# Kernel optimization log

Measured on AMD Instinct MI355X. Metric: run time of the kernel, lower is better.

Reference implementation:

```python
import jax, jax.numpy as jnp
import numpy as np
from jax import lax

V_VOX, T_PTS, D, H, W = 12000, 35, 10, 200, 176
EPS = 1e-5


def _bn(x, g, b, axes, shape):
    m = x.mean(axes, keepdims=True)
    v = x.var(axes, keepdims=True)  # biased var, matches torch BN training stats
    return g.reshape(shape) * (x - m) * lax.rsqrt(v + EPS) + b.reshape(shape)


def _conv3d(x, w, b):
    y = lax.conv_general_dilated(x, w, (1, 1, 1), 'SAME',
                                 dimension_numbers=('NCDHW', 'OIDHW', 'NCDHW'))
    return y + b[None, :, None, None, None]


def _conv2d(x, w, b):
    y = lax.conv_general_dilated(x, w, (1, 1), 'SAME',
                                 dimension_numbers=('NCHW', 'OIHW', 'NCHW'))
    return y + b[None, :, None, None]


def setup_inputs() -> dict:
    key = jax.random.key(0)
    ks = jax.random.split(key, 12)
    voxels = jax.random.normal(ks[0], (1, V_VOX, T_PTS, 4), jnp.float32)
    # unique voxel coordinates (the torch loop overwrites on duplicates; unique avoids ambiguity)
    rng = np.random.default_rng(0)
    flat = rng.choice(D * H * W, size=V_VOX, replace=False)
    z = flat // (H * W); rem = flat % (H * W)
    coords = jnp.asarray(np.stack([z, rem // W, rem % W], axis=1), dtype=jnp.int32)
    s = 0.05
    p = dict(
        w_lin=jax.random.normal(ks[1], (32, 4), jnp.float32) * s,
        b_lin=jnp.zeros((32,), jnp.float32),
        g_bn0=jnp.ones((32,), jnp.float32), be_bn0=jnp.zeros((32,), jnp.float32),
        w_c3a=jax.random.normal(ks[2], (64, 32, 3, 3, 3), jnp.float32) * s,
        b_c3a=jnp.zeros((64,), jnp.float32),
        g_bn1=jnp.ones((64,), jnp.float32), be_bn1=jnp.zeros((64,), jnp.float32),
        w_c3b=jax.random.normal(ks[3], (64, 64, 3, 3, 3), jnp.float32) * s,
        b_c3b=jnp.zeros((64,), jnp.float32),
        g_bn2=jnp.ones((64,), jnp.float32), be_bn2=jnp.zeros((64,), jnp.float32),
        w_r1=jax.random.normal(ks[4], (128, 64, 3, 3), jnp.float32) * s,
        b_r1=jnp.zeros((128,), jnp.float32),
        w_r2=jax.random.normal(ks[5], (8, 128, 1, 1), jnp.float32) * s,
        b_r2=jnp.zeros((8,), jnp.float32),
    )
    return dict(voxels=voxels, coords=coords, **p)


def reference(voxels, coords, w_lin, b_lin, g_bn0, be_bn0,
              w_c3a, b_c3a, g_bn1, be_bn1, w_c3b, b_c3b, g_bn2, be_bn2,
              w_r1, b_r1, w_r2, b_r2):
    B, V, T, C = voxels.shape
    # SimpleVFE: linear -> BN1d (batch stats) -> relu -> max over points
    h = voxels.reshape(B * V * T, C) @ w_lin.T + b_lin          # [BVT,32]
    h = jax.nn.relu(_bn(h, g_bn0, be_bn0, 0, (1, 32)))
    feats = h.reshape(B, V, T, 32).max(axis=2)                  # [B,V,32]
    # fused scatter into dense volume (replaces per-voxel python loop)
    volume = jnp.zeros((B, 32, D, H, W), voxels.dtype)
    volume = volume.at[0, :, coords[:, 0], coords[:, 1], coords[:, 2]].set(feats[0])
    # 3D backbone
    x = jax.nn.relu(_bn(_conv3d(volume, w_c3a, b_c3a), g_bn1, be_bn1, (0, 2, 3, 4), (1, 64, 1, 1, 1)))
    x = jax.nn.relu(_bn(_conv3d(x, w_c3b, b_c3b), g_bn2, be_bn2, (0, 2, 3, 4), (1, 64, 1, 1, 1)))
    x = x.mean(axis=2)                                          # collapse depth -> [B,64,H,W]
    # RPN head
    out = _conv2d(jax.nn.relu(_conv2d(x, w_r1, b_r1)), w_r2, b_r2)  # [B,8,H,W]
    box = jnp.concatenate([out[:, 0:3], jnp.exp(out[:, 3:6]),
                           jnp.tanh(out[:, 6:7]), jax.nn.sigmoid(out[:, 7:8])], axis=1)
    return box
```

## Files before the change

### kernel.cpp

```cpp
#include <hip/hip_runtime.h>
#include <math.h>

#define V_VOX 12000
#define T_PTS 35
#define DD 10
#define HH 200
#define WW 176
#define EPSV 1e-5f

#define DP 12
#define HP 202
#define WP 178
#define PPLN (HP * WP)
#define PVOX (DP * PPLN)
#define NPIX (DD * HH * WW)
#define HWPIX (HH * WW)

typedef _Float16 half_t;
typedef _Float16 f16x8 __attribute__((ext_vector_type(8)));
typedef float f32x4 __attribute__((ext_vector_type(4)));

#define WPA_OFF 0
#define WPB_OFF 110592
#define WPR1_OFF 331776
#define STATS_OFF 479232
#define FEATS_OFF 483328
#define VOLP_OFF 2019328
#define X1P_OFF 29633536
#define Y_OFF 84861952
#define PLANE_OFF 129917952
#define R1OUT_OFF 134520320

#define S_BN0S 0
#define S_BN0Q 32
#define S_BN1S 64
#define S_BN1Q 128
#define S_BN2S 192
#define S_BN2Q 256
#define C0A 320
#define C0B 352
#define C1A 384
#define C1B 448
#define C2A 512
#define C2B 576

__device__ __forceinline__ void gload16(const half_t* g, half_t* l) {
    __builtin_amdgcn_global_load_lds(
        (const __attribute__((address_space(1))) void*)g,
        (__attribute__((address_space(3))) void*)l, 16, 0, 0);
}

__global__ void k_pack(const float* __restrict__ w, half_t* __restrict__ wp,
                       int IC, int NT, int OC) {
    int id = blockIdx.x * 256 + threadIdx.x;
    int OCT = OC >> 4, KH = IC >> 5;
    int total = NT * KH * OCT * 512;
    if (id >= total) return;
    int j = id & 7;
    int lane = (id >> 3) & 63;
    int rest = id >> 9;
    int ot = rest % OCT; rest /= OCT;
    int kh = rest % KH;
    int tap = rest / KH;
    int oc = ot * 16 + (lane & 15);
    int ic = kh * 32 + (lane >> 4) * 8 + j;
    wp[id] = (half_t)w[(oc * IC + ic) * NT + tap];
}

__global__ void k_vfe_stats(const float4* __restrict__ vox, const float* __restrict__ w_lin,
                            const float* __restrict__ b_lin, float* __restrict__ S) {
    int tid = blockIdx.x * 256 + threadIdx.x;
    int c = threadIdx.x & 31;
    float4 w = ((const float4*)w_lin)[c];
    float bl = b_lin[c];
    float s = 0.f, q = 0.f;
    const int np = V_VOX * T_PTS;
    int stride = gridDim.x * 8;
    for (int p = tid >> 5; p < np; p += stride) {
        float4 v = vox[p];
        float d = v.x * w.x + v.y * w.y + v.z * w.z + v.w * w.w + bl;
        s += d;
        q += d * d;
    }
    s += __shfl_xor(s, 32);
    q += __shfl_xor(q, 32);
    if ((threadIdx.x & 63) < 32) {
        atomicAdd(&S[S_BN0S + c], s);
        atomicAdd(&S[S_BN0Q + c], q);
    }
}

__global__ void k_bn_final(const float* __restrict__ ss, const float* __restrict__ sq,
                           const float* __restrict__ g, const float* __restrict__ be,
                           float* __restrict__ ca, float* __restrict__ cb, int C, float invN) {
    int c = threadIdx.x;
    if (c >= C) return;
    float m = ss[c] * invN;
    float v = sq[c] * invN - m * m;
    float a = g[c] * rsqrtf(v + EPSV);
    ca[c] = a;
    cb[c] = be[c] - m * a;
}

__global__ void k_vfe_max(const float4* __restrict__ vox, const float* __restrict__ w_lin,
                          const float* __restrict__ b_lin, const float* __restrict__ ca,
                          const float* __restrict__ cb, float* __restrict__ feats) {
    int id = blockIdx.x * 256 + threadIdx.x;
    if (id >= V_VOX * 32) return;
    int c = id & 31;
    int v = id >> 5;
    float4 w = ((const float4*)w_lin)[c];
    float bl = b_lin[c], A = ca[c], B = cb[c];
    float m = 0.f;
    for (int t = 0; t < T_PTS; t++) {
        float4 p = vox[v * T_PTS + t];
        float d = p.x * w.x + p.y * w.y + p.z * w.z + p.w * w.w + bl;
        m = fmaxf(m, A * d + B);
    }
    feats[id] = m;
}

__global__ void k_scatter(const float* __restrict__ feats, const int* __restrict__ coords,
                          half_t* __restrict__ volp) {
    int id = blockIdx.x * 256 + threadIdx.x;
    if (id >= V_VOX * 32) return;
    int c = id & 31;
    int v = id >> 5;
    int z = coords[v * 3 + 0];
    int y = coords[v * 3 + 1];
    int x = coords[v * 3 + 2];
    volp[(((z + 1) * HP + (y + 1)) * WP + (x + 1)) * 32 + c] = (half_t)feats[id];
}

template <int KH, int DZ, int OCTP, bool RELU, bool STATS>
__global__ __launch_bounds__(256, 3) void k_conv(const half_t* __restrict__ in,
                                                 size_t khstride,
                                                 const half_t* __restrict__ wp,
                                                 const float* __restrict__ bias,
                                                 half_t* __restrict__ out,
                                                 float* __restrict__ ssum,
                                                 float* __restrict__ ssq) {
    constexpr int OC = OCTP * 16;
    constexpr int NS = DZ * KH;
    __shared__ __align__(16) half_t tA[2][24 * 512];

    const int tid = threadIdx.x;
    const int lane = tid & 63;
    const int wv = tid >> 6;
    const int x0 = blockIdx.x * 16;
    const int y0b = blockIdx.y * 16;
    const int bz = blockIdx.z;
    const int z0 = (DZ == 3) ? (bz >> 1) : 0;
    const int ocb = (DZ == 3) ? (bz & 1) * 2 : bz * 2;
    const int y0w = y0b + wv * 4;
    const bool valid = (y0w < HH);
    const int colc = lane & 15, grp = lane >> 4;

    unsigned gofsA[6];
#pragma unroll
    for (int i = 0; i < 6; ++i) {
        int run = wv + 4 * i;
        int c = run * 64 + lane;
        if (c > 1295) c = 1295;
        int pixhi = c >> 3, s = c & 7;
        int b = ((s >> 2) ^ (pixhi >> 1)) & 1;
        int q = ((s ^ b) & 1) | ((((s >> 1) ^ pixhi) & 1) << 1);
        int pix = pixhi * 2 + b;
        int row = pix / 18, px = pix - row * 18;
        int srow = y0b + row;
        if (srow > HP - 1) srow = HP - 1;
        gofsA[i] = (unsigned)((srow * WP + x0 + px) * 32 + q * 8);
    }

    f32x4 acc[4][2];
#pragma unroll
    for (int m = 0; m < 4; m++)
#pragma unroll
        for (int n = 0; n < 2; n++) acc[m][n] = (f32x4)(0.f);

    auto STAGEA = [&](int s, int buf) {
        const int dz = s / KH, kh = s % KH;
        const half_t* sl = in + (size_t)kh * khstride
                           + (size_t)(z0 + dz) * (DZ == 3 ? (size_t)PPLN * 32 : 0);
#pragma unroll
        for (int i = 0; i < 6; ++i) {
            int run = wv + 4 * i;
            gload16(sl + gofsA[i], &tA[buf][run * 512]);
        }
    };

    STAGEA(0, 0);

#pragma unroll 1
    for (int s = 0; s < NS; ++s) {
        const int dz = s / KH, kh = s % KH;
        f16x8 Breg[9][2];
#pragma unroll
        for (int tap = 0; tap < 9; ++tap)
#pragma unroll
            for (int n = 0; n < 2; ++n)
                Breg[tap][n] = *(const f16x8*)(wp
                    + (((size_t)(dz * 9 + tap) * KH + kh) * OCTP + ocb + n) * 512 + lane * 8);
        asm volatile("" ::: "memory");
        if (s + 1 < NS) {
            STAGEA(s + 1, (s + 1) & 1);
            asm volatile("s_waitcnt vmcnt(6)" ::: "memory");
        } else {
            asm volatile("s_waitcnt vmcnt(0)" ::: "memory");
        }
        __builtin_amdgcn_s_barrier();

        if (valid) {
            const int buf = s & 1;
#pragma unroll
            for (int dx = 0; dx < 3; ++dx) {
                f16x8 Af[6];
#pragma unroll
                for (int r = 0; r < 6; ++r) {
                    int pix = (wv * 4 + r) * 18 + colc + dx;
                    int ah = ((pix << 5) | (grp << 3)) ^ ((pix & 7) << 3);
                    Af[r] = *(const f16x8*)&tA[buf][ah];
                }
#pragma unroll
                for (int dy = 0; dy < 3; ++dy)
#pragma unroll
                    for (int m = 0; m < 4; ++m)
#pragma unroll
                        for (int n = 0; n < 2; ++n)
                            acc[m][n] = __builtin_amdgcn_mfma_f32_16x16x32_f16(
                                Af[dy + m], Breg[dy * 3 + dx][n], acc[m][n], 0, 0, 0);
            }
        }
        asm volatile("s_waitcnt lgkmcnt(0)" ::: "memory");
        __builtin_amdgcn_s_barrier();
    }

    if (!valid) return;
#pragma unroll
    for (int n = 0; n < 2; ++n) {
        int oc = (ocb + n) * 16 + colc;
        float bv = bias[oc];
        float s = 0.f, q = 0.f;
#pragma unroll
        for (int m = 0; m < 4; ++m) {
            int yy = y0w + m;
#pragma unroll
            for (int i = 0; i < 4; ++i) {
                int xx = x0 + grp * 4 + i;
                float v = acc[m][n][i] + bv;
                if (STATS) { s += v; q += v * v; }
                float w = RELU ? fmaxf(v, 0.f) : v;
                out[((size_t)(z0 * HH + yy) * WW + xx) * OC + oc] = (half_t)w;
            }
        }
        if (STATS) {
            s += __shfl_xor(s, 16); s += __shfl_xor(s, 32);
            q += __shfl_xor(q, 16); q += __shfl_xor(q, 32);
            if (lane < 16) {
                atomicAdd(&ssum[oc], s);
                atomicAdd(&ssq[oc], q);
            }
        }
    }
}

__global__ void k_activate(const half_t* __restrict__ y1, const float* __restrict__ ca,
                           const float* __restrict__ cb, half_t* __restrict__ xp) {
    int id = blockIdx.x * 256 + threadIdx.x;
    if (id >= PVOX * 8) return;
    int c0 = (id & 7) * 8;
    int pix = id >> 3;
    int zp = pix / PPLN;
    int rem = pix - zp * PPLN;
    int yp = rem / WP;
    int xq = rem - yp * WP;
    f16x8 o;
    if (zp >= 1 && zp <= DD && yp >= 1 && yp <= HH && xq >= 1 && xq <= WW) {
        size_t p = ((size_t)((zp - 1) * HH + (yp - 1)) * WW + (xq - 1));
        f16x8 v = *(const f16x8*)(y1 + p * 64 + c0);
#pragma unroll
        for (int j = 0; j < 8; j++)
            o[j] = (half_t)fmaxf(ca[c0 + j] * (float)v[j] + cb[c0 + j], 0.f);
    } else {
#pragma unroll
        for (int j = 0; j < 8; j++) o[j] = (half_t)0.f;
    }
    int khp = c0 >> 5;
    *(f16x8*)(xp + (size_t)khp * PVOX * 32 + (size_t)pix * 32 + (c0 & 31)) = o;
}

__global__ void k_depthmean(const half_t* __restrict__ y2, const float* __restrict__ ca,
                            const float* __restrict__ cb, half_t* __restrict__ plane) {
    int id = blockIdx.x * 256 + threadIdx.x;
    int c = id & 63;
    int pix = id >> 6;
    int yp = pix / WP;
    int xq = pix - yp * WP;
    float val = 0.f;
    if (yp >= 1 && yp <= HH && xq >= 1 && xq <= WW) {
        float A = ca[c], B = cb[c], s = 0.f;
        const half_t* base = y2 + ((size_t)(yp - 1) * WW + (xq - 1)) * 64 + c;
#pragma unroll
        for (int z = 0; z < DD; z++)
            s += fmaxf(A * (float)base[(size_t)z * HWPIX * 64] + B, 0.f);
        val = s * 0.1f;
    }
    int khp = c >> 5;
    plane[(size_t)khp * PPLN * 32 + (size_t)pix * 32 + (c & 31)] = (half_t)val;
}

__global__ void k_r2(const half_t* __restrict__ r1o, const float* __restrict__ w,
                     const float* __restrict__ bias, float* __restrict__ outp) {
    __shared__ float wsm[1024];
    for (int i = threadIdx.x; i < 1024; i += 256) wsm[i] = w[i];
    __syncthreads();
    int p = blockIdx.x * 256 + threadIdx.x;
    if (p >= HWPIX) return;
    float acc[8];
#pragma unroll
    for (int o = 0; o < 8; o++) acc[o] = bias[o];
    const half_t* rb = r1o + (size_t)p * 128;
#pragma unroll 4
    for (int icb = 0; icb < 128; icb += 8) {
        f16x8 v = *(const f16x8*)(rb + icb);
#pragma unroll
        for (int j = 0; j < 8; j++) {
            float vv = (float)v[j];
#pragma unroll
            for (int o = 0; o < 8; o++) acc[o] += vv * wsm[o * 128 + icb + j];
        }
    }
    outp[0 * HWPIX + p] = acc[0];
    outp[1 * HWPIX + p] = acc[1];
    outp[2 * HWPIX + p] = acc[2];
    outp[3 * HWPIX + p] = expf(acc[3]);
    outp[4 * HWPIX + p] = expf(acc[4]);
    outp[5 * HWPIX + p] = expf(acc[5]);
    outp[6 * HWPIX + p] = tanhf(acc[6]);
    outp[7 * HWPIX + p] = 1.f / (1.f + expf(-acc[7]));
}

extern "C" void kernel_launch(void* const* d_in, const int* in_sizes, int n_in,
                              void* d_out, int out_size, void* d_ws, size_t ws_size,
                              hipStream_t stream) {
    const float4* voxels = (const float4*)d_in[0];
    const int* coords = (const int*)d_in[1];
    const float* w_lin = (const float*)d_in[2];
    const float* b_lin = (const float*)d_in[3];
    const float* g_bn0 = (const float*)d_in[4];
    const float* be_bn0 = (const float*)d_in[5];
    const float* w_c3a = (const float*)d_in[6];
    const float* b_c3a = (const float*)d_in[7];
    const float* g_bn1 = (const float*)d_in[8];
    const float* be_bn1 = (const float*)d_in[9];
    const float* w_c3b = (const float*)d_in[10];
    const float* b_c3b = (const float*)d_in[11];
    const float* g_bn2 = (const float*)d_in[12];
    const float* be_bn2 = (const float*)d_in[13];
    const float* w_r1 = (const float*)d_in[14];
    const float* b_r1 = (const float*)d_in[15];
    const float* w_r2 = (const float*)d_in[16];
    const float* b_r2 = (const float*)d_in[17];

    char* ws = (char*)d_ws;
    half_t* wpA = (half_t*)(ws + WPA_OFF);
    half_t* wpB = (half_t*)(ws + WPB_OFF);
    half_t* wpR1 = (half_t*)(ws + WPR1_OFF);
    float* S = (float*)(ws + STATS_OFF);
    float* feats = (float*)(ws + FEATS_OFF);
    half_t* volp = (half_t*)(ws + VOLP_OFF);
    half_t* x1p = (half_t*)(ws + X1P_OFF);
    half_t* Y = (half_t*)(ws + Y_OFF);
    half_t* plane = (half_t*)(ws + PLANE_OFF);
    half_t* r1out = (half_t*)(ws + R1OUT_OFF);
    float* outp = (float*)d_out;

    hipMemsetAsync(S, 0, 320 * sizeof(float), stream);
    hipMemsetAsync(volp, 0, (size_t)PVOX * 32 * sizeof(half_t), stream);

    k_pack<<<216, 256, 0, stream>>>(w_c3a, wpA, 32, 27, 64);
    k_pack<<<432, 256, 0, stream>>>(w_c3b, wpB, 64, 27, 64);
    k_pack<<<288, 256, 0, stream>>>(w_r1, wpR1, 64, 9, 128);

    k_vfe_stats<<<512, 256, 0, stream>>>(voxels, w_lin, b_lin, S);
    k_bn_final<<<1, 64, 0, stream>>>(S + S_BN0S, S + S_BN0Q, g_bn0, be_bn0,
                                     S + C0A, S + C0B, 32, 1.f / 420000.f);
    k_vfe_max<<<1500, 256, 0, stream>>>(voxels, w_lin, b_lin, S + C0A, S + C0B, feats);
    k_scatter<<<1500, 256, 0, stream>>>(feats, coords, volp);

    k_conv<1, 3, 4, false, true><<<dim3(11, 13, 20), 256, 0, stream>>>(
        volp, 0, wpA, b_c3a, Y, S + S_BN1S, S + S_BN1Q);
    k_bn_final<<<1, 64, 0, stream>>>(S + S_BN1S, S + S_BN1Q, g_bn1, be_bn1,
                                     S + C1A, S + C1B, 64, 1.f / 352000.f);
    k_activate<<<13484, 256, 0, stream>>>(Y, S + C1A, S + C1B, x1p);

    k_conv<2, 3, 4, false, true><<<dim3(11, 13, 20), 256, 0, stream>>>(
        x1p, (size_t)PVOX * 32, wpB, b_c3b, Y, S + S_BN2S, S + S_BN2Q);
    k_bn_final<<<1, 64, 0, stream>>>(S + S_BN2S, S + S_BN2Q, g_bn2, be_bn2,
                                     S + C2A, S + C2B, 64, 1.f / 352000.f);

    k_depthmean<<<8989, 256, 0, stream>>>(Y, S + C2A, S + C2B, plane);

    k_conv<2, 1, 8, true, false><<<dim3(11, 13, 4), 256, 0, stream>>>(
        plane, (size_t)PPLN * 32, wpR1, b_r1, r1out, nullptr, nullptr);
    k_r2<<<138, 256, 0, stream>>>(r1out, w_r2, b_r2, outp);
}
```

Baseline: 461.7 us.

## Widen conv tile to 64 output channels per block and stream weights per dx

Each conv block now computes 4 output-channel tiles (64 channels) instead of 2, so the staged input tile in LDS is loaded once per block for all 64 channels, halving input staging traffic and the block count. Weight fragments are loaded per dx column in three register groups, interleaved with the MFMA work for the previous column, instead of all 9 taps up front. The doubled accumulator state raises register pressure, so launch bounds drop from 3 to 2 blocks per SM, which lowers occupancy and reduces the number of blocks available to fill the GPU.

```diff
diff --git a/kernel.cpp b/kernel.cpp
--- a/kernel.cpp
+++ b/kernel.cpp
@@ -133,7 +133,7 @@
 }
 
 template <int KH, int DZ, int OCTP, bool RELU, bool STATS>
-__global__ __launch_bounds__(256, 3) void k_conv(const half_t* __restrict__ in,
+__global__ __launch_bounds__(256, 2) void k_conv(const half_t* __restrict__ in,
                                                  size_t khstride,
                                                  const half_t* __restrict__ wp,
                                                  const float* __restrict__ bias,
@@ -150,8 +150,8 @@
     const int x0 = blockIdx.x * 16;
     const int y0b = blockIdx.y * 16;
     const int bz = blockIdx.z;
-    const int z0 = (DZ == 3) ? (bz >> 1) : 0;
-    const int ocb = (DZ == 3) ? (bz & 1) * 2 : bz * 2;
+    const int z0 = (DZ == 3) ? bz : 0;
+    const int ocb = (DZ == 3) ? 0 : bz * 4;
     const int y0w = y0b + wv * 4;
     const bool valid = (y0w < HH);
     const int colc = lane & 15, grp = lane >> 4;
@@ -172,11 +172,11 @@
         gofsA[i] = (unsigned)((srow * WP + x0 + px) * 32 + q * 8);
     }
 
-    f32x4 acc[4][2];
+    f32x4 acc[4][4];
 #pragma unroll
     for (int m = 0; m < 4; m++)
 #pragma unroll
-        for (int n = 0; n < 2; n++) acc[m][n] = (f32x4)(0.f);
+        for (int n = 0; n < 4; n++) acc[m][n] = (f32x4)(0.f);
 
     auto STAGEA = [&](int s, int buf) {
         const int dz = s / KH, kh = s % KH;
@@ -188,19 +188,40 @@
             gload16(sl + gofsA[i], &tA[buf][run * 512]);
         }
     };
+    auto LOADB = [&](f16x8 (&B)[3][4], int dz, int kh, int dx) {
+#pragma unroll
+        for (int dy = 0; dy < 3; ++dy)
+#pragma unroll
+            for (int n = 0; n < 4; ++n)
+                B[dy][n] = *(const f16x8*)(wp
+                    + (((size_t)(dz * 9 + dy * 3 + dx) * KH + kh) * OCTP + ocb + n) * 512
+                    + lane * 8);
+    };
+    auto CDX = [&](int buf, int dx, f16x8 (&B)[3][4]) {
+        f16x8 Af[6];
+#pragma unroll
+        for (int r = 0; r < 6; ++r) {
+            int pix = (wv * 4 + r) * 18 + colc + dx;
+            int ah = ((pix << 5) | (grp << 3)) ^ ((pix & 7) << 3);
+            Af[r] = *(const f16x8*)&tA[buf][ah];
+        }
+#pragma unroll
+        for (int dy = 0; dy < 3; ++dy)
+#pragma unroll
+            for (int m = 0; m < 4; ++m)
+#pragma unroll
+                for (int n = 0; n < 4; ++n)
+                    acc[m][n] = __builtin_amdgcn_mfma_f32_16x16x32_f16(
+                        Af[dy + m], B[dy][n], acc[m][n], 0, 0, 0);
+    };
 
     STAGEA(0, 0);
 
 #pragma unroll 1
     for (int s = 0; s < NS; ++s) {
         const int dz = s / KH, kh = s % KH;
-        f16x8 Breg[9][2];
-#pragma unroll
-        for (int tap = 0; tap < 9; ++tap)
-#pragma unroll
-            for (int n = 0; n < 2; ++n)
-                Breg[tap][n] = *(const f16x8*)(wp
-                    + (((size_t)(dz * 9 + tap) * KH + kh) * OCTP + ocb + n) * 512 + lane * 8);
+        f16x8 B0[3][4], B1[3][4], B2[3][4];
+        LOADB(B0, dz, kh, 0);
         asm volatile("" ::: "memory");
         if (s + 1 < NS) {
             STAGEA(s + 1, (s + 1) & 1);
@@ -210,34 +231,20 @@
         }
         __builtin_amdgcn_s_barrier();
 
-        if (valid) {
-            const int buf = s & 1;
-#pragma unroll
-            for (int dx = 0; dx < 3; ++dx) {
-                f16x8 Af[6];
-#pragma unroll
-                for (int r = 0; r < 6; ++r) {
-                    int pix = (wv * 4 + r) * 18 + colc + dx;
-                    int ah = ((pix << 5) | (grp << 3)) ^ ((pix & 7) << 3);
-                    Af[r] = *(const f16x8*)&tA[buf][ah];
-                }
-#pragma unroll
-                for (int dy = 0; dy < 3; ++dy)
-#pragma unroll
-                    for (int m = 0; m < 4; ++m)
-#pragma unroll
-                        for (int n = 0; n < 2; ++n)
-                            acc[m][n] = __builtin_amdgcn_mfma_f32_16x16x32_f16(
-                                Af[dy + m], Breg[dy * 3 + dx][n], acc[m][n], 0, 0, 0);
-            }
-        }
+        const int buf = s & 1;
+        LOADB(B1, dz, kh, 1);
+        if (valid) CDX(buf, 0, B0);
+        LOADB(B2, dz, kh, 2);
+        if (valid) CDX(buf, 1, B1);
+        if (valid) CDX(buf, 2, B2);
+
         asm volatile("s_waitcnt lgkmcnt(0)" ::: "memory");
         __builtin_amdgcn_s_barrier();
     }
 
     if (!valid) return;
 #pragma unroll
-    for (int n = 0; n < 2; ++n) {
+    for (int n = 0; n < 4; ++n) {
         int oc = (ocb + n) * 16 + colc;
         float bv = bias[oc];
         float s = 0.f, q = 0.f;
@@ -388,20 +395,20 @@
     k_vfe_max<<<1500, 256, 0, stream>>>(voxels, w_lin, b_lin, S + C0A, S + C0B, feats);
     k_scatter<<<1500, 256, 0, stream>>>(feats, coords, volp);
 
-    k_conv<1, 3, 4, false, true><<<dim3(11, 13, 20), 256, 0, stream>>>(
+    k_conv<1, 3, 4, false, true><<<dim3(11, 13, 10), 256, 0, stream>>>(
         volp, 0, wpA, b_c3a, Y, S + S_BN1S, S + S_BN1Q);
     k_bn_final<<<1, 64, 0, stream>>>(S + S_BN1S, S + S_BN1Q, g_bn1, be_bn1,
                                      S + C1A, S + C1B, 64, 1.f / 352000.f);
     k_activate<<<13484, 256, 0, stream>>>(Y, S + C1A, S + C1B, x1p);
 
-    k_conv<2, 3, 4, false, true><<<dim3(11, 13, 20), 256, 0, stream>>>(
+    k_conv<2, 3, 4, false, true><<<dim3(11, 13, 10), 256, 0, stream>>>(
         x1p, (size_t)PVOX * 32, wpB, b_c3b, Y, S + S_BN2S, S + S_BN2Q);
     k_bn_final<<<1, 64, 0, stream>>>(S + S_BN2S, S + S_BN2Q, g_bn2, be_bn2,
                                      S + C2A, S + C2B, 64, 1.f / 352000.f);
 
     k_depthmean<<<8989, 256, 0, stream>>>(Y, S + C2A, S + C2B, plane);
 
-    k_conv<2, 1, 8, true, false><<<dim3(11, 13, 4), 256, 0, stream>>>(
+    k_conv<2, 1, 8, true, false><<<dim3(11, 13, 2), 256, 0, stream>>>(
         plane, (size_t)PPLN * 32, wpR1, b_r1, r1out, nullptr, nullptr);
     k_r2<<<138, 256, 0, stream>>>(r1out, w_r2, b_r2, outp);
 }
```

New measurement: 491.6 us. 6.5% more time.
